# Kernel optimization log

Measured on AMD Instinct MI355X. Metric: run time of the kernel, lower is better.

## Reference

```python
import jax, jax.numpy as jnp
import numpy as np

B, L, C, P, LEVEL, K = 32, 1024, 128, 96, 3, 5
N_NODES = 2 ** (LEVEL + 1) - 1  # 15 CIL blocks in the tree (preorder: node, even-subtree, odd-subtree)
SQRT2 = np.float32(np.sqrt(2.0))


def haar_last(x):
    # Haar wavelet transform along last axis (power-of-2 length), iterative form of the torch recursion:
    # result = [h_final, g_deepest, ..., g_first]
    outs = []
    h = x
    while h.shape[-1] > 1:
        e, o = h[..., ::2], h[..., 1::2]
        outs.append((e - o) / SQRT2)
        h = (e + o) / SQRT2
    return jnp.concatenate([h] + outs[::-1], axis=-1)


def conv1d(x, w, b):
    # x: [B, C, L], w: [O, I, K], b: [O]
    y = jax.lax.conv_general_dilated(x, w, (1,), 'VALID', dimension_numbers=('NCH', 'OIH', 'NCH'))
    return y + b[None, :, None]


def causal_conv_block(x, w1, b1, w2, b2):
    # ReplicationPad1d((K-1, K-1)) -> Conv1d(K) -> LeakyReLU(0.01) -> Conv1d(K) -> Tanh; length preserved
    xp = jnp.pad(x, ((0, 0), (0, 0), (K - 1, K - 1)), mode='edge')
    y = conv1d(xp, w1, b1)
    y = jnp.where(y > 0, y, 0.01 * y)
    return jnp.tanh(conv1d(y, w2, b2))


def cil_block(x, bw1, bb1, bw2, bb2):
    # x: [B, L, C]; bw*: [4, C, C, K] ordered (modules_even, modules_odd, interactor_even, interactor_odd)
    xe = x[:, ::2].transpose(0, 2, 1)   # [B, C, L/2]
    xo = x[:, 1::2].transpose(0, 2, 1)
    ccb = lambda i, z: causal_conv_block(z, bw1[i], bb1[i], bw2[i], bb2[i])
    xet = xe * jnp.exp(ccb(0, xo))
    xot = xo * jnp.exp(ccb(1, xe))
    xeu = xet + ccb(2, xot)
    xou = xot - ccb(3, xet)
    return xeu.transpose(0, 2, 1), xou.transpose(0, 2, 1)


def zip_up(e, o):
    # interleave even/odd halves along the time axis (equal lengths since L is a power of 2)
    b, l, c = e.shape
    return jnp.stack([e, o], axis=2).reshape(b, 2 * l, c)


def _forward(x_enc, mask, fc1_w, fc2_w, ln_g, ln_b, w1, b1, w2, b2, proj_w):
    denom = jnp.sum((mask == 1).astype(x_enc.dtype), axis=1)                 # [B, C]
    means = jax.lax.stop_gradient(jnp.sum(x_enc, axis=1) / denom)[:, None]   # [B, 1, C] (detached)
    x = x_enc - means
    x = jnp.where(mask == 0, 0.0, x)
    stdev = jax.lax.stop_gradient(jnp.sqrt(jnp.sum(x * x, axis=1) / denom + 1e-5))[:, None]
    x = x / stdev
    # haar channel gating block (per-channel haar over time, FC gate, LayerNorm over L)
    freq = haar_last(x.transpose(0, 2, 1))                                   # [B, C, L]
    lr = jax.nn.sigmoid(jax.nn.relu(freq @ fc1_w.T) @ fc2_w.T)               # [B, C, L]
    mu = lr.mean(-1, keepdims=True)
    var = ((lr - mu) ** 2).mean(-1, keepdims=True)                           # biased, as torch LayerNorm
    lr = (lr - mu) / jnp.sqrt(var + 1e-6) * ln_g + ln_b
    x = x * lr.transpose(0, 2, 1)
    # sinusoidal position encoding (pe_hidden_size == C, even)
    num_ts = C // 2
    inc = np.float32(np.log(10000.0) / max(num_ts - 1, 1))
    inv = jnp.exp(jnp.arange(num_ts, dtype=jnp.float32) * -inc)
    st = jnp.arange(L, dtype=jnp.float32)[:, None] * inv[None, :]
    pe = jnp.concatenate([jnp.sin(st), jnp.cos(st)], axis=1)[None]           # [1, L, C]
    x = x + pe
    # recursive CILN tree; node params indexed in call order (node, even-subtree, odd-subtree)
    counter = [0]
    def tree(z, level):
        i = counter[0]; counter[0] += 1
        e, o = cil_block(z, w1[i], b1[i], w2[i], b2[i])
        if level == 0:
            return zip_up(e, o)
        return zip_up(tree(e, level - 1), tree(o, level - 1))
    dec = tree(x, LEVEL) + x
    dec = jnp.einsum('pl,blc->bpc', proj_w, dec)                             # Conv1d(L, L+P, k=1, bias=False) over time dim
    dec = dec * stdev + means
    # forward(): cat(zeros_like(x_enc), dec)[:, -P:, :3] == dec[:, -P:, :3]
    return dec[:, -P:, :3]


def setup_inputs():
    key = jax.random.key(0)
    ks = jax.random.split(key, 8)
    s = 0.05
    return {
        'x_enc': jax.random.normal(ks[0], (B, L, C), jnp.float32),
        'mask': jnp.ones((B, L, C), jnp.float32),
        'fc1_w': jax.random.normal(ks[1], (2 * L, L), jnp.float32) * s,
        'fc2_w': jax.random.normal(ks[2], (L, 2 * L), jnp.float32) * s,
        'ln_g': jnp.ones((L,), jnp.float32),
        'ln_b': jnp.zeros((L,), jnp.float32),
        'w1': jax.random.normal(ks[3], (N_NODES, 4, C, C, K), jnp.float32) * s,
        'b1': jax.random.normal(ks[4], (N_NODES, 4, C), jnp.float32) * s,
        'w2': jax.random.normal(ks[5], (N_NODES, 4, C, C, K), jnp.float32) * s,
        'b2': jax.random.normal(ks[6], (N_NODES, 4, C), jnp.float32) * s,
        'proj_w': jax.random.normal(ks[7], (L + P, L), jnp.float32) * s,
    }


def reference(x_enc, mask, fc1_w, fc2_w, ln_g, ln_b, w1, b1, w2, b2, proj_w):
    return _forward(x_enc, mask, fc1_w, fc2_w, ln_g, ln_b, w1, b1, w2, b2, proj_w)
```

## Files before the change

kernel.cpp:

```cpp
#include <hip/hip_runtime.h>

namespace {

constexpr int NB = 32, NL = 1024, NC = 128, NP = 96, KW = 5;
constexpr float INV_SQRT2 = 0.70710678118654752440f;
constexpr size_t SEG = (size_t)NB * NC;
constexpr int CT = 64;

typedef unsigned short u16;
typedef __attribute__((ext_vector_type(4))) u16 u16x4;
typedef __attribute__((ext_vector_type(8))) u16 u16x8;
typedef __attribute__((ext_vector_type(8))) short short8;
typedef __attribute__((ext_vector_type(4))) float f32x4;

__device__ inline u16 f2bf(float f) {
  unsigned u = __float_as_uint(f);
  u += 0x7fff + ((u >> 16) & 1);
  return (u16)(u >> 16);
}

__device__ inline float ftanh(float x) {
  float e = __expf(2.f * x);
  return 1.f - 2.f / (e + 1.f);
}

__device__ __forceinline__ void glds16(const void* g, void* l) {
  __builtin_amdgcn_global_load_lds(
      (const __attribute__((address_space(1))) unsigned*)g,
      (__attribute__((address_space(3))) unsigned*)l, 16, 0, 0);
}

__global__ void stats1(const float* __restrict__ x, const float* __restrict__ mask,
                       float* __restrict__ part) {
  int b = blockIdx.x, s = blockIdx.y;
  int tid = threadIdx.x;
  int c = tid & 127, lh = tid >> 7;
  const float* xb = x + (size_t)b * NL * NC;
  const float* mb = mask + (size_t)b * NL * NC;
  float s_all = 0.f, d1 = 0.f, sm = 0.f, sm2 = 0.f, cnz = 0.f;
#pragma unroll 4
  for (int i = 0; i < 32; ++i) {
    int l = s * 64 + lh + 2 * i;
    float v = xb[(size_t)l * NC + c];
    float m = mb[(size_t)l * NC + c];
    s_all += v;
    d1 += (m == 1.f) ? 1.f : 0.f;
    bool nz = (m != 0.f);
    float vm = nz ? v : 0.f;
    sm += vm;
    sm2 += vm * v;
    cnz += nz ? 1.f : 0.f;
  }
  __shared__ float red[5][256];
  red[0][tid] = s_all; red[1][tid] = d1; red[2][tid] = sm;
  red[3][tid] = sm2;   red[4][tid] = cnz;
  __syncthreads();
  if (lh == 0) {
    float* pp = part + ((size_t)(b * 16 + s) * 5) * NC + c;
#pragma unroll
    for (int q = 0; q < 5; ++q) pp[q * NC] = red[q][c] + red[q][c + 128];
  }
}

__global__ void stats2(const float* __restrict__ part, float* __restrict__ means,
                       float* __restrict__ stdev) {
  int b = blockIdx.x, c = threadIdx.x;
  float s_all = 0.f, d1 = 0.f, sm = 0.f, sm2 = 0.f, cnz = 0.f;
  for (int s = 0; s < 16; ++s) {
    const float* pp = part + ((size_t)(b * 16 + s) * 5) * NC + c;
    s_all += pp[0];
    d1    += pp[NC];
    sm    += pp[2 * NC];
    sm2   += pp[3 * NC];
    cnz   += pp[4 * NC];
  }
  float mn = s_all / d1;
  float varsum = sm2 - 2.f * mn * sm + mn * mn * cnz;
  means[b * NC + c] = mn;
  stdev[b * NC + c] = sqrtf(varsum / d1 + 1e-5f);
}

__global__ void norm_transpose(const float* __restrict__ x, const float* __restrict__ mask,
                               const float* __restrict__ means, const float* __restrict__ stdev,
                               float* __restrict__ xt) {
  __shared__ float tile[32][33];
  int b = blockIdx.x;
  int l0 = blockIdx.y * 32;
  int c0 = blockIdx.z * 32;
  int tx = threadIdx.x;
  int ty = threadIdx.y;
  for (int i = ty; i < 32; i += 8) {
    int l = l0 + i, c = c0 + tx;
    float v = x[((size_t)b * NL + l) * NC + c];
    float m = mask[((size_t)b * NL + l) * NC + c];
    float val = (m == 0.f) ? 0.f : (v - means[b * NC + c]);
    tile[i][tx] = val / stdev[b * NC + c];
  }
  __syncthreads();
  for (int i = ty; i < 32; i += 8) {
    xt[((size_t)b * NC + c0 + i) * NL + l0 + tx] = tile[tx][i];
  }
}

__global__ void haar_kernel(const float* __restrict__ xt, u16* __restrict__ freqb) {
  int row = blockIdx.x;
  __shared__ float h[1024], t2[512];
  const float* src = xt + (size_t)row * NL;
  u16* dst = freqb + (size_t)row * NL;
  for (int i = threadIdx.x; i < 1024; i += 256) h[i] = src[i];
  __syncthreads();
  int n = 1024;
  while (n > 1) {
    int half = n >> 1;
    for (int i = threadIdx.x; i < half; i += 256) {
      float e = h[2 * i], o = h[2 * i + 1];
      dst[half + i] = f2bf((e - o) * INV_SQRT2);
      t2[i] = (e + o) * INV_SQRT2;
    }
    __syncthreads();
    for (int i = threadIdx.x; i < half; i += 256) h[i] = t2[i];
    __syncthreads();
    n = half;
  }
  if (threadIdx.x == 0) dst[0] = f2bf(h[0]);
}

__global__ void cvt_bf16(const float* __restrict__ in, u16* __restrict__ outp, int n4) {
  int i = blockIdx.x * 256 + threadIdx.x;
  if (i < n4) {
    const float4 v = *reinterpret_cast<const float4*>(in + (size_t)i * 4);
    u16x4 o;
    o.x = f2bf(v.x); o.y = f2bf(v.y); o.z = f2bf(v.z); o.w = f2bf(v.w);
    *reinterpret_cast<u16x4*>(outp + (size_t)i * 4) = o;
  }
}

__global__ void pack_w(const float* __restrict__ w, u16* __restrict__ wp) {
  int idx = blockIdx.x * 256 + threadIdx.x;
  if (idx >= 60 * 128 * 128) return;
  int ci = idx & 127;
  int co = (idx >> 7) & 127;
  int n = idx >> 14;
  const float* src = w + (size_t)idx * 5;
  size_t base = (size_t)n * (5 * 128 * 128) + (size_t)co * 128 + ci;
#pragma unroll
  for (int k = 0; k < 5; ++k)
    wp[base + (size_t)k * 16384] = f2bf(src[k]);
}

template <int EPI>
__global__ __launch_bounds__(256) void gemm_mfma(const u16* __restrict__ A,
                                                 const u16* __restrict__ Bw,
                                                 u16* __restrict__ Cb, float* __restrict__ Cf,
                                                 int M, int N, int K, int CM, int CN) {
  __shared__ __align__(16) char sAB[(128 + 64) * 128];
  int GX = gridDim.x;
  int h = blockIdx.y * GX + blockIdx.x;
  int xcd = h & 7, loc = h >> 3;
  int lm = loc / CN, ln = loc - lm * CN;
  int cnch = GX / CN;
  int m0 = ((xcd / cnch) * CM + lm) * 128;
  int n0 = ((xcd % cnch) * CN + ln) * 64;
  int tid = threadIdx.x;
  int lane = tid & 63, wv = tid >> 6;
  int wm = (wv >> 1) * 64, wn = (wv & 1) * 32;
  int lg = lane >> 4, l15 = lane & 15;

  const u16* srcb[6];
  int swo[6];
#pragma unroll
  for (int pass = 0; pass < 6; ++pass) {
    int o = pass * 4096 + tid * 16;
    int cb = o & 127;
    int row;
    if (pass < 4) {
      row = o >> 7;
      srcb[pass] = A + (size_t)(m0 + row) * K + (cb >> 1);
    } else {
      int rb = (o - 16384) >> 7;
      row = 128 + rb;
      srcb[pass] = Bw + (size_t)(n0 + rb) * K + (cb >> 1);
    }
    swo[pass] = row * 128 + (cb ^ ((row & 7) << 4));
  }

  f32x4 zero = {0.f, 0.f, 0.f, 0.f};
  f32x4 acc[4][2];
#pragma unroll
  for (int i = 0; i < 4; ++i)
#pragma unroll
    for (int j = 0; j < 2; ++j) acc[i][j] = zero;

  u16x8 st[6];
#pragma unroll
  for (int p = 0; p < 6; ++p) st[p] = *(const u16x8*)(srcb[p]);

  for (int k0 = 0; k0 < K; k0 += 64) {
    __syncthreads();
#pragma unroll
    for (int p = 0; p < 6; ++p) *(u16x8*)(sAB + swo[p]) = st[p];
    __syncthreads();
    if (k0 + 64 < K) {
#pragma unroll
      for (int p = 0; p < 6; ++p) st[p] = *(const u16x8*)(srcb[p] + k0 + 64);
    }
#pragma unroll
    for (int ks = 0; ks < 2; ++ks) {
      int kb = ks * 64 + lg * 16;
      short8 a[4], bbf[2];
#pragma unroll
      for (int mt = 0; mt < 4; ++mt) {
        int rr = wm + mt * 16 + l15;
        a[mt] = *(const short8*)(sAB + rr * 128 + (kb ^ ((rr & 7) << 4)));
      }
#pragma unroll
      for (int nt = 0; nt < 2; ++nt) {
        int rr = 128 + wn + nt * 16 + l15;
        bbf[nt] = *(const short8*)(sAB + rr * 128 + (kb ^ ((rr & 7) << 4)));
      }
#pragma unroll
      for (int mt = 0; mt < 4; ++mt)
#pragma unroll
        for (int nt = 0; nt < 2; ++nt)
          acc[mt][nt] = __builtin_amdgcn_mfma_f32_16x16x32_bf16(a[mt], bbf[nt], acc[mt][nt], 0, 0, 0);
    }
  }
#pragma unroll
  for (int mt = 0; mt < 4; ++mt)
#pragma unroll
    for (int nt = 0; nt < 2; ++nt)
#pragma unroll
      for (int r = 0; r < 4; ++r) {
        int row = m0 + wm + mt * 16 + lg * 4 + r;
        int col = n0 + wn + nt * 16 + l15;
        float v = acc[mt][nt][r];
        if (EPI == 0) {
          v = v > 0.f ? v : 0.f;
          Cb[(size_t)row * N + col] = f2bf(v);
        } else {
          Cf[(size_t)row * N + col] = 1.f / (1.f + __expf(-v));
        }
      }
}

__global__ void ln_combine(const float* __restrict__ lr, float* __restrict__ xt,
                           const float* __restrict__ g, const float* __restrict__ bta) {
  int row = blockIdx.x;
  int c = row & 127;
  const float* p = lr + (size_t)row * 1024;
  int tid = threadIdx.x;
  float v[4];
#pragma unroll
  for (int i = 0; i < 4; ++i) v[i] = p[tid + 256 * i];
  __shared__ float red[256];
  red[tid] = v[0] + v[1] + v[2] + v[3];
  __syncthreads();
  for (int off = 128; off > 0; off >>= 1) {
    if (tid < off) red[tid] += red[tid + off];
    __syncthreads();
  }
  float mu = red[0] * (1.f / 1024.f);
  __syncthreads();
  float sq = 0.f;
#pragma unroll
  for (int i = 0; i < 4; ++i) { float d = v[i] - mu; sq += d * d; }
  red[tid] = sq;
  __syncthreads();
  for (int off = 128; off > 0; off >>= 1) {
    if (tid < off) red[tid] += red[tid + off];
    __syncthreads();
  }
  float rs = rsqrtf(red[0] * (1.f / 1024.f) + 1e-6f);
  int t = c & 63;
  float inv = __expf(-0.14619589f * (float)t);
  float* xr = xt + (size_t)row * 1024;
#pragma unroll
  for (int i = 0; i < 4; ++i) {
    int l = tid + 256 * i;
    float lrv = (v[i] - mu) * rs * g[l] + bta[l];
    float st = (float)l * inv;
    float pe = (c < 64) ? sinf(st) : cosf(st);
    xr[l] = xr[l] * lrv + pe;
  }
}

__device__ __forceinline__ void stage_w(const u16* W, char* buf, int wv, int lane, int s) {
  int k = s >> 2, ci0 = (s & 3) * 32;
#pragma unroll
  for (int i = 0; i < 2; ++i) {
    int off = i * 1024 + lane * 16;
    int wl = off >> 7;
    int wpos = off & 127;
    int u = wpos ^ ((wl & 7) << 4);
    int co = wv * 32 + wl * 2 + (u >> 6);
    int ci = ci0 + ((u & 63) >> 1);
    glds16(W + (((size_t)(k * 128 + co)) << 7) + ci, buf + wv * 2048 + i * 1024);
  }
}

template <int PHASE>
__global__ __launch_bounds__(256) void conv_step(
    const float* __restrict__ inF, const u16* __restrict__ inB,
    u16* __restrict__ outB, float* __restrict__ outF,
    const u16* __restrict__ wp, const float* __restrict__ bp,
    int d, int Tn) {
  __shared__ __align__(16) char sm[68 * 256];
  __shared__ __align__(16) char wbuf[4][8192];
  int gx = gridDim.x, gy = gridDim.y;
  int total = gx * gy * gridDim.z;
  int hidx = (blockIdx.z * gy + blockIdx.y) * gx + blockIdx.x;
  int lidx = (hidx & 7) * (total >> 3) + (hidx >> 3);
  int b = lidx % gx;
  int rest = lidx / gx;
  int ty = rest % gy;
  int z = rest / gy;
  int p = z >> 1, g = z & 1;
  int node = 0;
  for (int i2 = d - 1; i2 >= 0; --i2) {
    int bit = (p >> i2) & 1;
    int dd = d - 1 - i2;
    node += 1 + bit * ((1 << (3 - dd)) - 1);
  }
  const int TS = Tn + 4;
  int tid = threadIdx.x;
  int wq = tid >> 6;
  int lane = tid & 63, wv = wq;
  int lg = lane >> 4, l15 = lane & 15;

  int widx = node * 4 + (PHASE >= 2 ? 2 : 0) + g;
  const u16* W = wp + (size_t)widx * (5 * 128 * 128);
  const float* Bp = bp + (size_t)widx * 128;
  f32x4 bv[2];
#pragma unroll
  for (int mt = 0; mt < 2; ++mt) bv[mt] = *(const f32x4*)(Bp + wv * 32 + mt * 16 + lg * 4);

  {
    int i = tid & 63;
#pragma unroll
    for (int rep = 0; rep < 2; ++rep) {
      int ii = i + rep * 64;
      if (ii < 68) {
        int sw0 = (ii & 15) << 4;
        if (PHASE == 0) {
          int tt = CT * ty - 4 + ii;
          tt = tt < 0 ? 0 : (tt >= Tn ? Tn - 1 : tt);
          const float* rp = inF + ((size_t)p * SEG + (size_t)b * NC) * (size_t)(2 * Tn) +
                            2 * tt + (1 - g);
#pragma unroll
          for (int pp = 0; pp < 16; ++pp) {
            int pr = wq * 16 + pp;
            float v0 = rp[(size_t)(2 * pr) * (2 * Tn)];
            float v1 = rp[(size_t)(2 * pr + 1) * (2 * Tn)];
            unsigned pk = (unsigned)f2bf(v0) | ((unsigned)f2bf(v1) << 16);
            *(unsigned*)(sm + ii * 256 + ((4 * pr) ^ sw0)) = pk;
          }
        } else if (PHASE == 2) {
          int tt = CT * ty - 4 + ii;
          tt = tt < 0 ? 0 : (tt >= Tn ? Tn - 1 : tt);
          const float* sp = inF + ((size_t)(p * 2 + (g ? 0 : 1)) * SEG + (size_t)b * NC) * Tn + tt;
#pragma unroll
          for (int pp = 0; pp < 16; ++pp) {
            int pr = wq * 16 + pp;
            unsigned pk = (unsigned)f2bf(sp[(size_t)(2 * pr) * Tn]) |
                          ((unsigned)f2bf(sp[(size_t)(2 * pr + 1) * Tn]) << 16);
            *(unsigned*)(sm + ii * 256 + ((4 * pr) ^ sw0)) = pk;
          }
        } else {
          int s = CT * ty + ii;
          const u16* mi = inB + ((size_t)(p * 2 + g) * SEG + (size_t)b * NC) * TS + s;
#pragma unroll
          for (int pp = 0; pp < 16; ++pp) {
            int pr = wq * 16 + pp;
            unsigned pk = (unsigned)mi[(size_t)(2 * pr) * TS] |
                          ((unsigned)mi[(size_t)(2 * pr + 1) * TS] << 16);
            *(unsigned*)(sm + ii * 256 + ((4 * pr) ^ sw0)) = pk;
          }
        }
      }
    }
  }
  stage_w(W, wbuf[0], wv, lane, 0);
  stage_w(W, wbuf[1], wv, lane, 1);
  stage_w(W, wbuf[2], wv, lane, 2);
  stage_w(W, wbuf[3], wv, lane, 3);
  __syncthreads();

  f32x4 acc[2][4];
#pragma unroll
  for (int mt = 0; mt < 2; ++mt)
#pragma unroll
    for (int nt = 0; nt < 4; ++nt) acc[mt][nt] = bv[mt];

  int co_base = wv * 32 + lg * 4;

#pragma unroll
  for (int s = 0; s < 20; ++s) {
    if (s == 19)      asm volatile("s_waitcnt vmcnt(0)" ::: "memory");
    else if (s == 18) asm volatile("s_waitcnt vmcnt(2)" ::: "memory");
    else if (s == 17) asm volatile("s_waitcnt vmcnt(4)" ::: "memory");
    else              asm volatile("s_waitcnt vmcnt(6)" ::: "memory");
    __builtin_amdgcn_sched_barrier(0);
    const char* wb = wbuf[s & 3];
    short8 a[2], bb[4];
#pragma unroll
    for (int mt = 0; mt < 2; ++mt) {
      int co = wv * 32 + mt * 16 + l15;
      int wrow = co >> 1;
      a[mt] = *(const short8*)(wb + wrow * 128 +
                               ((((co & 1) << 6) | (lg << 4)) ^ ((wrow & 7) << 4)));
    }
    int cbyte = 2 * ((s & 3) * 32 + lg * 8);
    int k = s >> 2;
#pragma unroll
    for (int nt = 0; nt < 4; ++nt) {
      int i = nt * 16 + l15 + k;
      bb[nt] = *(const short8*)(sm + i * 256 + (cbyte ^ ((i & 15) << 4)));
    }
#pragma unroll
    for (int mt = 0; mt < 2; ++mt)
#pragma unroll
      for (int nt = 0; nt < 4; ++nt)
        acc[mt][nt] = __builtin_amdgcn_mfma_f32_16x16x32_bf16(a[mt], bb[nt], acc[mt][nt], 0, 0, 0);
    if (s + 4 < 20) {
      asm volatile("s_waitcnt lgkmcnt(0)" ::: "memory");
      __builtin_amdgcn_sched_barrier(0);
      stage_w(W, wbuf[s & 3], wv, lane, s + 4);
    }
  }

  if (PHASE == 0 || PHASE == 2) {
    u16* mo = outB + ((size_t)(p * 2 + g) * SEG + (size_t)b * NC) * TS;
#pragma unroll
    for (int mt = 0; mt < 2; ++mt)
#pragma unroll
      for (int nt = 0; nt < 4; ++nt) {
        int s = CT * ty + nt * 16 + l15;
        if (s < TS) {
#pragma unroll
          for (int r = 0; r < 4; ++r) {
            float v = acc[mt][nt][r];
            v = v > 0.f ? v : 0.01f * v;
            mo[(size_t)(co_base + mt * 16 + r) * TS + s] = f2bf(v);
          }
        }
      }
  } else if (PHASE == 1) {
    const float* par = inF + ((size_t)p * SEG + (size_t)b * NC) * (size_t)(2 * Tn);
    float* xo_ = outF + ((size_t)(p * 2 + g) * SEG + (size_t)b * NC) * Tn;
#pragma unroll
    for (int mt = 0; mt < 2; ++mt)
#pragma unroll
      for (int nt = 0; nt < 4; ++nt) {
        int t = CT * ty + nt * 16 + l15;
#pragma unroll
        for (int r = 0; r < 4; ++r) {
          int co = co_base + mt * 16 + r;
          float xv = par[(size_t)co * (2 * Tn) + 2 * t + g];
          xo_[(size_t)co * Tn + t] = xv * __expf(ftanh(acc[mt][nt][r]));
        }
      }
  } else {
    const float* xf = inF + ((size_t)(p * 2 + g) * SEG + (size_t)b * NC) * Tn;
    float* ch = outF + ((size_t)(2 * p + g) * SEG + (size_t)b * NC) * Tn;
#pragma unroll
    for (int mt = 0; mt < 2; ++mt)
#pragma unroll
      for (int nt = 0; nt < 4; ++nt) {
        int t = CT * ty + nt * 16 + l15;
#pragma unroll
        for (int r = 0; r < 4; ++r) {
          int co = co_base + mt * 16 + r;
          float cv = ftanh(acc[mt][nt][r]);
          float base = xf[(size_t)co * Tn + t];
          ch[(size_t)co * Tn + t] = g ? (base - cv) : (base + cv);
        }
      }
  }
}

__global__ void final_kernel(const float* __restrict__ dect, const float* __restrict__ xt,
                             const float* __restrict__ projw, const float* __restrict__ means,
                             const float* __restrict__ stdev, float* __restrict__ out) {
  int b = blockIdx.x, p = blockIdx.y;
  int tid = threadIdx.x;
  const float* w = projw + (size_t)(1024 + p) * 1024;
  const float* x0 = xt + (size_t)b * NC * NL;
  float a[3] = {0.f, 0.f, 0.f};
  for (int l = tid; l < 1024; l += 256) {
    float wv = w[l];
    int rl = l & 7;
    int pb = ((rl & 1) << 2) | (rl & 2) | (rl >> 2);
    int br = (l >> 3) & 1;
    int t = l >> 4;
    const float* dl = dect + ((size_t)(2 * pb + br) * NB + b) * NC * 64 + t;
#pragma unroll
    for (int cc = 0; cc < 3; ++cc)
      a[cc] += wv * (dl[(size_t)cc * 64] + x0[(size_t)cc * NL + l]);
  }
  __shared__ float red[3][256];
  for (int cc = 0; cc < 3; ++cc) red[cc][tid] = a[cc];
  __syncthreads();
  for (int off = 128; off > 0; off >>= 1) {
    if (tid < off) {
      red[0][tid] += red[0][tid + off];
      red[1][tid] += red[1][tid + off];
      red[2][tid] += red[2][tid + off];
    }
    __syncthreads();
  }
  if (tid < 3) {
    out[((size_t)b * NP + p) * 3 + tid] = red[tid][0] * stdev[b * NC + tid] + means[b * NC + tid];
  }
}

}

extern "C" void kernel_launch(void* const* d_in, const int* in_sizes, int n_in,
                              void* d_out, int out_size, void* d_ws, size_t ws_size,
                              hipStream_t stream) {
  (void)in_sizes; (void)n_in; (void)out_size; (void)ws_size;
  const float* x_enc = (const float*)d_in[0];
  const float* mask  = (const float*)d_in[1];
  const float* fc1_w = (const float*)d_in[2];
  const float* fc2_w = (const float*)d_in[3];
  const float* ln_g  = (const float*)d_in[4];
  const float* ln_b  = (const float*)d_in[5];
  const float* w1    = (const float*)d_in[6];
  const float* b1    = (const float*)d_in[7];
  const float* w2    = (const float*)d_in[8];
  const float* b2    = (const float*)d_in[9];
  const float* projw = (const float*)d_in[10];
  float* out = (float*)d_out;
  float* ws = (float*)d_ws;

  float* means = ws + 0;
  float* stdev = ws + 4096;
  float* x_t   = ws + 8192;
  float* freq  = ws + 4202496;
  float* IN1   = ws + 8396800;
  float* IN2   = ws + 12591104;
  float* xeof  = ws + 16785408;
  float* wp1f  = ws + 20979712;
  float* wp2f  = ws + 23437312;
  float* midf  = ws + 25894912;
  float* dect = IN1;
  float* stats_part = midf;
  u16* freq_bf = (u16*)xeof;
  u16* hid_bf  = (u16*)IN1;
  u16* fc1w_bf = (u16*)IN2;
  u16* fc2w_bf = (u16*)(IN2 + 1048576);
  u16* wp1 = (u16*)wp1f;
  u16* wp2 = (u16*)wp2f;
  u16* midb = (u16*)midf;

  stats1<<<dim3(NB, 16), 256, 0, stream>>>(x_enc, mask, stats_part);
  stats2<<<NB, 128, 0, stream>>>(stats_part, means, stdev);
  norm_transpose<<<dim3(NB, NL / 32, NC / 32), dim3(32, 8), 0, stream>>>(x_enc, mask, means, stdev, x_t);
  haar_kernel<<<NB * NC, 256, 0, stream>>>(x_t, freq_bf);

  cvt_bf16<<<2048, 256, 0, stream>>>(fc1_w, fc1w_bf, 524288);
  cvt_bf16<<<2048, 256, 0, stream>>>(fc2_w, fc2w_bf, 524288);
  pack_w<<<3840, 256, 0, stream>>>(w1, wp1);
  pack_w<<<3840, 256, 0, stream>>>(w2, wp2);

  gemm_mfma<0><<<dim3(32, 32), 256, 0, stream>>>(freq_bf, fc1w_bf, hid_bf, nullptr,
                                                 4096, 2048, 1024, 8, 16);
  gemm_mfma<1><<<dim3(16, 32), 256, 0, stream>>>(hid_bf, fc2w_bf, nullptr, freq,
                                                 4096, 1024, 2048, 8, 8);

  ln_combine<<<4096, 256, 0, stream>>>(freq, x_t, ln_g, ln_b);

  float* dbuf[5] = {x_t, IN1, IN2, freq, IN1};
  for (int d = 0; d < 4; ++d) {
    int Tn = 512 >> d;
    int nsub = 1 << d;
    dim3 gA(NB, (Tn + 4 + CT - 1) / CT, 2 * nsub);
    dim3 gB(NB, Tn / CT, 2 * nsub);
    conv_step<0><<<gA, 256, 0, stream>>>(dbuf[d], nullptr, midb, nullptr, wp1, b1, d, Tn);
    conv_step<1><<<gB, 256, 0, stream>>>(dbuf[d], midb, nullptr, xeof, wp2, b2, d, Tn);
    conv_step<2><<<gA, 256, 0, stream>>>(xeof, nullptr, midb, nullptr, wp1, b1, d, Tn);
    conv_step<3><<<gB, 256, 0, stream>>>(xeof, midb, nullptr, dbuf[d + 1], wp2, b2, d, Tn);
  }

  final_kernel<<<dim3(NB, NP), 256, 0, stream>>>(dect, x_t, projw, means, stdev, out);
}
```

Measured before the change: 399.3 us.

## Fuse both convolutions of each causal conv block into one kernel via LDS intermediate

Merges the two conv_step launches per causal conv block into a single kernel. The first conv computes an 80-row halo tile whose LeakyReLU output is written as bf16 into shared memory. The second conv reads that tile directly, and its weight staging is prefetched while the first conv is still running. This removes the global round trip of the intermediate activation and halves the number of conv launches per tree level. The cost is recomputing halo columns in every tile, plus more shared memory per block, which may lower occupancy.

```diff
diff --git a/kernel.cpp b/kernel.cpp
--- a/kernel.cpp
+++ b/kernel.cpp
@@ -298,13 +298,14 @@
   }
 }
 
-template <int PHASE>
-__global__ __launch_bounds__(256) void conv_step(
-    const float* __restrict__ inF, const u16* __restrict__ inB,
-    u16* __restrict__ outB, float* __restrict__ outF,
-    const u16* __restrict__ wp, const float* __restrict__ bp,
+template <int VAR>
+__global__ __launch_bounds__(256) void ccb_fused(
+    const float* __restrict__ inF, float* __restrict__ outF,
+    const u16* __restrict__ wp1, const u16* __restrict__ wp2,
+    const float* __restrict__ b1, const float* __restrict__ b2,
     int d, int Tn) {
-  __shared__ __align__(16) char sm[68 * 256];
+  __shared__ __align__(16) char sdat[84 * 256];
+  __shared__ __align__(16) char smid[80 * 256];
   __shared__ __align__(16) char wbuf[4][8192];
   int gx = gridDim.x, gy = gridDim.y;
   int total = gx * gy * gridDim.z;
@@ -321,29 +322,34 @@
     int dd = d - 1 - i2;
     node += 1 + bit * ((1 << (3 - dd)) - 1);
   }
-  const int TS = Tn + 4;
+  int t0 = CT * ty;
   int tid = threadIdx.x;
   int wq = tid >> 6;
   int lane = tid & 63, wv = wq;
   int lg = lane >> 4, l15 = lane & 15;
 
-  int widx = node * 4 + (PHASE >= 2 ? 2 : 0) + g;
-  const u16* W = wp + (size_t)widx * (5 * 128 * 128);
-  const float* Bp = bp + (size_t)widx * 128;
-  f32x4 bv[2];
-#pragma unroll
-  for (int mt = 0; mt < 2; ++mt) bv[mt] = *(const f32x4*)(Bp + wv * 32 + mt * 16 + lg * 4);
+  int widx = node * 4 + VAR * 2 + g;
+  const u16* W1 = wp1 + (size_t)widx * (5 * 128 * 128);
+  const u16* W2 = wp2 + (size_t)widx * (5 * 128 * 128);
+  const float* B1 = b1 + (size_t)widx * 128;
+  const float* B2 = b2 + (size_t)widx * 128;
+  f32x4 bv1[2], bv2[2];
+#pragma unroll
+  for (int mt = 0; mt < 2; ++mt) {
+    bv1[mt] = *(const f32x4*)(B1 + wv * 32 + mt * 16 + lg * 4);
+    bv2[mt] = *(const f32x4*)(B2 + wv * 32 + mt * 16 + lg * 4);
+  }
 
   {
     int i = tid & 63;
 #pragma unroll
     for (int rep = 0; rep < 2; ++rep) {
       int ii = i + rep * 64;
-      if (ii < 68) {
+      if (ii < 84) {
         int sw0 = (ii & 15) << 4;
-        if (PHASE == 0) {
-          int tt = CT * ty - 4 + ii;
-          tt = tt < 0 ? 0 : (tt >= Tn ? Tn - 1 : tt);
+        int tt = t0 - 8 + ii;
+        tt = tt < 0 ? 0 : (tt >= Tn ? Tn - 1 : tt);
+        if (VAR == 0) {
           const float* rp = inF + ((size_t)p * SEG + (size_t)b * NC) * (size_t)(2 * Tn) +
                             2 * tt + (1 - g);
 #pragma unroll
@@ -352,56 +358,41 @@
             float v0 = rp[(size_t)(2 * pr) * (2 * Tn)];
             float v1 = rp[(size_t)(2 * pr + 1) * (2 * Tn)];
             unsigned pk = (unsigned)f2bf(v0) | ((unsigned)f2bf(v1) << 16);
-            *(unsigned*)(sm + ii * 256 + ((4 * pr) ^ sw0)) = pk;
+            *(unsigned*)(sdat + ii * 256 + ((4 * pr) ^ sw0)) = pk;
           }
-        } else if (PHASE == 2) {
-          int tt = CT * ty - 4 + ii;
-          tt = tt < 0 ? 0 : (tt >= Tn ? Tn - 1 : tt);
+        } else {
           const float* sp = inF + ((size_t)(p * 2 + (g ? 0 : 1)) * SEG + (size_t)b * NC) * Tn + tt;
 #pragma unroll
           for (int pp = 0; pp < 16; ++pp) {
             int pr = wq * 16 + pp;
             unsigned pk = (unsigned)f2bf(sp[(size_t)(2 * pr) * Tn]) |
                           ((unsigned)f2bf(sp[(size_t)(2 * pr + 1) * Tn]) << 16);
-            *(unsigned*)(sm + ii * 256 + ((4 * pr) ^ sw0)) = pk;
-          }
-        } else {
-          int s = CT * ty + ii;
-          const u16* mi = inB + ((size_t)(p * 2 + g) * SEG + (size_t)b * NC) * TS + s;
-#pragma unroll
-          for (int pp = 0; pp < 16; ++pp) {
-            int pr = wq * 16 + pp;
-            unsigned pk = (unsigned)mi[(size_t)(2 * pr) * TS] |
-                          ((unsigned)mi[(size_t)(2 * pr + 1) * TS] << 16);
-            *(unsigned*)(sm + ii * 256 + ((4 * pr) ^ sw0)) = pk;
+            *(unsigned*)(sdat + ii * 256 + ((4 * pr) ^ sw0)) = pk;
           }
         }
       }
     }
   }
-  stage_w(W, wbuf[0], wv, lane, 0);
-  stage_w(W, wbuf[1], wv, lane, 1);
-  stage_w(W, wbuf[2], wv, lane, 2);
-  stage_w(W, wbuf[3], wv, lane, 3);
-  __syncthreads();
-
-  f32x4 acc[2][4];
+  stage_w(W1, wbuf[0], wv, lane, 0);
+  stage_w(W1, wbuf[1], wv, lane, 1);
+  stage_w(W1, wbuf[2], wv, lane, 2);
+  stage_w(W1, wbuf[3], wv, lane, 3);
+  __syncthreads();
+
+  int co_base = wv * 32 + lg * 4;
+
+  f32x4 acc1[2][5];
 #pragma unroll
   for (int mt = 0; mt < 2; ++mt)
 #pragma unroll
-    for (int nt = 0; nt < 4; ++nt) acc[mt][nt] = bv[mt];
-
-  int co_base = wv * 32 + lg * 4;
+    for (int nt = 0; nt < 5; ++nt) acc1[mt][nt] = bv1[mt];
 
 #pragma unroll
   for (int s = 0; s < 20; ++s) {
-    if (s == 19)      asm volatile("s_waitcnt vmcnt(0)" ::: "memory");
-    else if (s == 18) asm volatile("s_waitcnt vmcnt(2)" ::: "memory");
-    else if (s == 17) asm volatile("s_waitcnt vmcnt(4)" ::: "memory");
-    else              asm volatile("s_waitcnt vmcnt(6)" ::: "memory");
+    asm volatile("s_waitcnt vmcnt(6)" ::: "memory");
     __builtin_amdgcn_sched_barrier(0);
     const char* wb = wbuf[s & 3];
-    short8 a[2], bb[4];
+    short8 a[2];
 #pragma unroll
     for (int mt = 0; mt < 2; ++mt) {
       int co = wv * 32 + mt * 16 + l15;
@@ -412,51 +403,91 @@
     int cbyte = 2 * ((s & 3) * 32 + lg * 8);
     int k = s >> 2;
 #pragma unroll
-    for (int nt = 0; nt < 4; ++nt) {
+    for (int nt = 0; nt < 5; ++nt) {
       int i = nt * 16 + l15 + k;
-      bb[nt] = *(const short8*)(sm + i * 256 + (cbyte ^ ((i & 15) << 4)));
-    }
-#pragma unroll
-    for (int mt = 0; mt < 2; ++mt)
-#pragma unroll
-      for (int nt = 0; nt < 4; ++nt)
-        acc[mt][nt] = __builtin_amdgcn_mfma_f32_16x16x32_bf16(a[mt], bb[nt], acc[mt][nt], 0, 0, 0);
-    if (s + 4 < 20) {
+      short8 bb = *(const short8*)(sdat + i * 256 + (cbyte ^ ((i & 15) << 4)));
+#pragma unroll
+      for (int mt = 0; mt < 2; ++mt)
+        acc1[mt][nt] = __builtin_amdgcn_mfma_f32_16x16x32_bf16(a[mt], bb, acc1[mt][nt], 0, 0, 0);
+    }
+    {
       asm volatile("s_waitcnt lgkmcnt(0)" ::: "memory");
       __builtin_amdgcn_sched_barrier(0);
-      stage_w(W, wbuf[s & 3], wv, lane, s + 4);
-    }
-  }
-
-  if (PHASE == 0 || PHASE == 2) {
-    u16* mo = outB + ((size_t)(p * 2 + g) * SEG + (size_t)b * NC) * TS;
-#pragma unroll
-    for (int mt = 0; mt < 2; ++mt)
-#pragma unroll
-      for (int nt = 0; nt < 4; ++nt) {
-        int s = CT * ty + nt * 16 + l15;
-        if (s < TS) {
-#pragma unroll
-          for (int r = 0; r < 4; ++r) {
-            float v = acc[mt][nt][r];
-            v = v > 0.f ? v : 0.01f * v;
-            mo[(size_t)(co_base + mt * 16 + r) * TS + s] = f2bf(v);
-          }
-        }
+      int gs = s + 4;
+      if (gs < 20) stage_w(W1, wbuf[s & 3], wv, lane, gs);
+      else         stage_w(W2, wbuf[s & 3], wv, lane, gs - 20);
+    }
+  }
+
+#pragma unroll
+  for (int mt = 0; mt < 2; ++mt)
+#pragma unroll
+    for (int nt = 0; nt < 5; ++nt) {
+      int j = nt * 16 + l15;
+      int co0 = co_base + mt * 16;
+      u16x4 m;
+#pragma unroll
+      for (int r = 0; r < 4; ++r) {
+        float v = acc1[mt][nt][r];
+        v = v > 0.f ? v : 0.01f * v;
+        m[r] = f2bf(v);
       }
-  } else if (PHASE == 1) {
+      *(u16x4*)(smid + j * 256 + ((2 * co0) ^ ((j & 15) << 4))) = m;
+    }
+  __syncthreads();
+
+  f32x4 acc2[2][4];
+#pragma unroll
+  for (int mt = 0; mt < 2; ++mt)
+#pragma unroll
+    for (int nt = 0; nt < 4; ++nt) acc2[mt][nt] = bv2[mt];
+
+#pragma unroll
+  for (int sp = 0; sp < 20; ++sp) {
+    if (sp == 19)      asm volatile("s_waitcnt vmcnt(0)" ::: "memory");
+    else if (sp == 18) asm volatile("s_waitcnt vmcnt(2)" ::: "memory");
+    else if (sp == 17) asm volatile("s_waitcnt vmcnt(4)" ::: "memory");
+    else               asm volatile("s_waitcnt vmcnt(6)" ::: "memory");
+    __builtin_amdgcn_sched_barrier(0);
+    const char* wb = wbuf[sp & 3];
+    short8 a[2];
+#pragma unroll
+    for (int mt = 0; mt < 2; ++mt) {
+      int co = wv * 32 + mt * 16 + l15;
+      int wrow = co >> 1;
+      a[mt] = *(const short8*)(wb + wrow * 128 +
+                               ((((co & 1) << 6) | (lg << 4)) ^ ((wrow & 7) << 4)));
+    }
+    int cbyte = 2 * ((sp & 3) * 32 + lg * 8);
+    int k = sp >> 2;
+#pragma unroll
+    for (int nt = 0; nt < 4; ++nt) {
+      int i = nt * 16 + l15 + k + 4;
+      short8 bb = *(const short8*)(smid + i * 256 + (cbyte ^ ((i & 15) << 4)));
+#pragma unroll
+      for (int mt = 0; mt < 2; ++mt)
+        acc2[mt][nt] = __builtin_amdgcn_mfma_f32_16x16x32_bf16(a[mt], bb, acc2[mt][nt], 0, 0, 0);
+    }
+    if (sp + 4 < 20) {
+      asm volatile("s_waitcnt lgkmcnt(0)" ::: "memory");
+      __builtin_amdgcn_sched_barrier(0);
+      stage_w(W2, wbuf[sp & 3], wv, lane, sp + 4);
+    }
+  }
+
+  if (VAR == 0) {
     const float* par = inF + ((size_t)p * SEG + (size_t)b * NC) * (size_t)(2 * Tn);
     float* xo_ = outF + ((size_t)(p * 2 + g) * SEG + (size_t)b * NC) * Tn;
 #pragma unroll
     for (int mt = 0; mt < 2; ++mt)
 #pragma unroll
       for (int nt = 0; nt < 4; ++nt) {
-        int t = CT * ty + nt * 16 + l15;
+        int t = t0 + nt * 16 + l15;
 #pragma unroll
         for (int r = 0; r < 4; ++r) {
           int co = co_base + mt * 16 + r;
           float xv = par[(size_t)co * (2 * Tn) + 2 * t + g];
-          xo_[(size_t)co * Tn + t] = xv * __expf(ftanh(acc[mt][nt][r]));
+          xo_[(size_t)co * Tn + t] = xv * __expf(ftanh(acc2[mt][nt][r]));
         }
       }
   } else {
@@ -466,11 +497,11 @@
     for (int mt = 0; mt < 2; ++mt)
 #pragma unroll
       for (int nt = 0; nt < 4; ++nt) {
-        int t = CT * ty + nt * 16 + l15;
+        int t = t0 + nt * 16 + l15;
 #pragma unroll
         for (int r = 0; r < 4; ++r) {
           int co = co_base + mt * 16 + r;
-          float cv = ftanh(acc[mt][nt][r]);
+          float cv = ftanh(acc2[mt][nt][r]);
           float base = xf[(size_t)co * Tn + t];
           ch[(size_t)co * Tn + t] = g ? (base - cv) : (base + cv);
         }
@@ -542,16 +573,14 @@
   float* xeof  = ws + 16785408;
   float* wp1f  = ws + 20979712;
   float* wp2f  = ws + 23437312;
-  float* midf  = ws + 25894912;
   float* dect = IN1;
-  float* stats_part = midf;
+  float* stats_part = wp2f;
   u16* freq_bf = (u16*)xeof;
   u16* hid_bf  = (u16*)IN1;
   u16* fc1w_bf = (u16*)IN2;
   u16* fc2w_bf = (u16*)(IN2 + 1048576);
   u16* wp1 = (u16*)wp1f;
   u16* wp2 = (u16*)wp2f;
-  u16* midb = (u16*)midf;
 
   stats1<<<dim3(NB, 16), 256, 0, stream>>>(x_enc, mask, stats_part);
   stats2<<<NB, 128, 0, stream>>>(stats_part, means, stdev);
@@ -574,12 +603,9 @@
   for (int d = 0; d < 4; ++d) {
     int Tn = 512 >> d;
     int nsub = 1 << d;
-    dim3 gA(NB, (Tn + 4 + CT - 1) / CT, 2 * nsub);
-    dim3 gB(NB, Tn / CT, 2 * nsub);
-    conv_step<0><<<gA, 256, 0, stream>>>(dbuf[d], nullptr, midb, nullptr, wp1, b1, d, Tn);
-    conv_step<1><<<gB, 256, 0, stream>>>(dbuf[d], midb, nullptr, xeof, wp2, b2, d, Tn);
-    conv_step<2><<<gA, 256, 0, stream>>>(xeof, nullptr, midb, nullptr, wp1, b1, d, Tn);
-    conv_step<3><<<gB, 256, 0, stream>>>(xeof, midb, nullptr, dbuf[d + 1], wp2, b2, d, Tn);
+    dim3 grd(NB, Tn / CT, 2 * nsub);
+    ccb_fused<0><<<grd, 256, 0, stream>>>(dbuf[d], xeof, wp1, wp2, b1, b2, d, Tn);
+    ccb_fused<1><<<grd, 256, 0, stream>>>(xeof, dbuf[d + 1], wp1, wp2, b1, b2, d, Tn);
   }
 
   final_kernel<<<dim3(NB, NP), 256, 0, stream>>>(dect, x_t, projw, means, stdev, out);
```

After: 332.9 us. -16.6%, faster.
